# Performance work log

Hardware: AMD Instinct MI355X
Metric: run time of the kernel (lower is better)

The kernel has to match this reference:

```python
import jax, jax.numpy as jnp
import numpy as np

ADMP = 16  # admp_channel


def _backbone(x, Wc, bc):
    # Conv2d(3->256, k=3, stride=2, pad=1) + ReLU stands in for feature_backbone
    y = jax.lax.conv_general_dilated(x, Wc, window_strides=(2, 2),
                                     padding=((1, 1), (1, 1)),
                                     dimension_numbers=('NCHW', 'OIHW', 'NCHW'))
    return jax.nn.relu(y + bc[None, :, None, None])


def _feature_select(feat, k):
    # AdaptiveMaxPool2d(k, return_indices=True) on feat.sum(1); H,W divisible by k
    B, C, H, W = feat.shape
    bh, bw = H // k, W // k
    resp = feat.sum(1)  # [B,H,W]
    r = resp.reshape(B, k, bh, k, bw).transpose(0, 1, 3, 2, 4).reshape(B, k, k, bh * bw)
    loc = jnp.argmax(r, axis=-1)            # local flat index in each bh*bw block
    lr, lc = loc // bw, loc % bw
    rows = jnp.arange(k)[None, :, None] * bh + lr   # [B,k,k]
    cols = jnp.arange(k)[None, None, :] * bw + lc
    return (rows * W + cols).reshape(B, k * k)      # flat indices into H*W


def _mlp(x, W1, b1, W2, b2):
    # Linear -> ReLU -> (Dropout eval = identity) -> Linear
    return jax.nn.relu(x @ W1 + b1) @ W2 + b2


def reference(xA, xB, Wconv, bconv, W1r, b1r, W2r, b2r, W1c, b1c, W2c, b2c):
    fA = _backbone(xA, Wconv, bconv)  # [B,C,H,W]
    fB = _backbone(xB, Wconv, bconv)
    B, C, H, W = fA.shape
    N = H * W
    idxA = _feature_select(fA, ADMP)                       # [B,K]
    fA_flat = fA.reshape(B, C, N)
    fB_flat = fB.reshape(B, C, N)
    desc = jnp.take_along_axis(fA_flat, idxA[:, None, :], axis=2)  # [B,C,K]
    # ||a-b||^2 = ||a||^2 - 2 a.b + ||b||^2 ; fused batched kNN
    dist = ((desc ** 2).sum(1)[:, :, None]
            - 2.0 * jnp.einsum('bck,bcn->bkn', desc, fB_flat)
            + (fB_flat ** 2).sum(1)[:, None, :])           # [B,K,N]
    minidx = jnp.argmin(dist, axis=-1)                     # [B,K]
    # original uses high (==width here since H==W) for both div and mod
    row_A, col_A = idxA // H, idxA % H
    row_B, col_B = minidx // H, minidx % H
    drow = (row_B - row_A).astype(jnp.float32)             # [B,K]
    dcol = (col_A - col_B).astype(jnp.float32)
    out_drow = _mlp(drow, W1r, b1r, W2r, b2r)              # [B,1]
    out_dcol = _mlp(dcol, W1c, b1c, W2c, b2c)
    return jnp.concatenate([out_drow, out_dcol], axis=1)   # [B,2]


def setup_inputs() -> dict:
    key = jax.random.key(0)
    ks = jax.random.split(key, 8)
    K2 = ADMP * ADMP
    return {
        'xA': jax.random.normal(ks[0], (4, 3, 256, 256), jnp.float32),
        'xB': jax.random.normal(ks[1], (4, 3, 256, 256), jnp.float32),
        'Wconv': jax.random.normal(ks[2], (256, 3, 3, 3), jnp.float32) * 0.1,
        'bconv': jnp.zeros((256,), jnp.float32),
        'W1r': jax.random.normal(ks[3], (K2, K2 // 2), jnp.float32) * 0.05,
        'b1r': jnp.zeros((K2 // 2,), jnp.float32),
        'W2r': jax.random.normal(ks[4], (K2 // 2, 1), jnp.float32) * 0.05,
        'b2r': jnp.zeros((1,), jnp.float32),
        'W1c': jax.random.normal(ks[5], (K2, K2 // 2), jnp.float32) * 0.05,
        'b1c': jnp.zeros((K2 // 2,), jnp.float32),
        'W2c': jax.random.normal(ks[6], (K2 // 2, 1), jnp.float32) * 0.05,
        'b2c': jnp.zeros((1,), jnp.float32),
    }
```

## Files before the change

kernel.cpp:

```cpp
#include <hip/hip_runtime.h>
#include <stdint.h>

constexpr int NB   = 4;
constexpr int CIN  = 3;
constexpr int HIN  = 256;
constexpr int COUT = 256;
constexpr int HF   = 128;
constexpr int NF   = HF * HF;
constexpr int KADM = 16;
constexpr int KK   = KADM * KADM;
constexpr int HID  = 128;
constexpr int DFB  = 65536;
constexpr int PX   = 32;
constexpr int NT   = NF / PX;

typedef unsigned short ushort_t;
typedef __attribute__((ext_vector_type(8))) _Float16 f16x8;
typedef __attribute__((ext_vector_type(4))) float    f32x4;

__device__ inline unsigned long long shfl_xor_u64(unsigned long long v, int m) {
    unsigned lo = __shfl_xor((unsigned)v, m, 64);
    unsigned hi = __shfl_xor((unsigned)(v >> 32), m, 64);
    return ((unsigned long long)hi << 32) | lo;
}
__device__ inline unsigned long long shfl_down_u64(unsigned long long v, int off) {
    unsigned lo = __shfl_down((unsigned)v, off, 64);
    unsigned hi = __shfl_down((unsigned)(v >> 32), off, 64);
    return ((unsigned long long)hi << 32) | lo;
}
__device__ inline unsigned long long u64min(unsigned long long a, unsigned long long b) {
    return a < b ? a : b;
}
__device__ inline ushort_t f16bits(_Float16 h) { return __builtin_bit_cast(ushort_t, h); }

__device__ inline int swz(int pix, int c) {
    return pix * 256 + ((((c >> 3) ^ (pix & 7)) << 3) | (c & 7));
}

__device__ inline int dfoff(int w, int chunk, int j, int lane) {
    return (((w * 8 + chunk) * 4 + j) * 64 + lane) * 8;
}

__global__ __launch_bounds__(256) void prep_kernel(
        const float* __restrict__ W, ushort_t* __restrict__ WFh, ushort_t* __restrict__ WFl)
{
    int co = threadIdx.x;
    int w = co >> 6, j = (co >> 4) & 3, la = co & 15;
    #pragma unroll
    for (int q = 0; q < 32; ++q) {
        float v = (q < 27) ? W[co * 27 + q] : 0.f;
        _Float16 h = (_Float16)v;
        _Float16 l = (_Float16)(v - (float)h);
        int lg = q >> 3, e = q & 7;
        int off = ((w * 4 + j) * 64 + lg * 16 + la) * 8 + e;
        WFh[off] = f16bits(h);
        WFl[off] = f16bits(l);
    }
}

__global__ __launch_bounds__(256) void convA_kernel(
        const float* __restrict__ xA,
        const ushort_t* __restrict__ WFh, const ushort_t* __restrict__ WFl,
        const float* __restrict__ bias, float* __restrict__ resp)
{
    __shared__ float    pS[CIN][3][132];
    __shared__ ushort_t Ah[64][40];
    __shared__ ushort_t Al[64][40];
    __shared__ float    redS[4][64];

    int tile = blockIdx.x;
    int b    = blockIdx.y;
    int oh   = tile >> 1;
    int ow0  = (tile & 1) << 6;
    const float* x = xA + (size_t)b * CIN * HIN * HIN;
    int tid = threadIdx.x;

    for (int i = tid; i < CIN * 3 * 129; i += 256) {
        int ci = i / (3 * 129);
        int r2 = i % (3 * 129);
        int kh = r2 / 129, c = r2 % 129;
        int gr = 2 * oh - 1 + kh, gc = 2 * ow0 - 1 + c;
        float v = 0.f;
        if (gr >= 0 && gr < HIN && gc >= 0 && gc < HIN)
            v = x[(size_t)ci * HIN * HIN + (size_t)gr * HIN + gc];
        pS[ci][kh][c] = v;
    }
    __syncthreads();

    {
        int n = tid >> 2, qg = tid & 3;
        unsigned uh[4], ul[4];
        #pragma unroll
        for (int e2 = 0; e2 < 4; ++e2) {
            ushort_t hh[2], ll[2];
            #pragma unroll
            for (int s = 0; s < 2; ++s) {
                int q = qg * 8 + e2 * 2 + s;
                float v = 0.f;
                if (q < 27) {
                    int ci = q / 9, r = (q % 9) / 3, kw = q % 3;
                    v = pS[ci][r][2 * n + kw];
                }
                _Float16 h = (_Float16)v;
                _Float16 l = (_Float16)(v - (float)h);
                hh[s] = f16bits(h); ll[s] = f16bits(l);
            }
            uh[e2] = (unsigned)hh[0] | ((unsigned)hh[1] << 16);
            ul[e2] = (unsigned)ll[0] | ((unsigned)ll[1] << 16);
        }
        *(uint4*)&Ah[n][qg * 8] = *(uint4*)uh;
        *(uint4*)&Al[n][qg * 8] = *(uint4*)ul;
    }
    __syncthreads();

    int lane = tid & 63, w = tid >> 6;
    int la = lane & 15, lg = lane >> 4;
    int wbase = w * 64;

    float bj[4];
    #pragma unroll
    for (int j = 0; j < 4; ++j) bj[j] = bias[wbase + j * 16 + la];

    f16x8 ah[4], al[4], bh[4], bl[4];
    #pragma unroll
    for (int i = 0; i < 4; ++i) {
        ah[i] = *(const f16x8*)&Ah[i * 16 + la][lg * 8];
        al[i] = *(const f16x8*)&Al[i * 16 + la][lg * 8];
    }
    #pragma unroll
    for (int j = 0; j < 4; ++j) {
        int off = ((w * 4 + j) * 64 + lane) * 8;
        bh[j] = *(const f16x8*)&WFh[off];
        bl[j] = *(const f16x8*)&WFl[off];
    }

    f32x4 acc[4][4];
    #pragma unroll
    for (int i = 0; i < 4; ++i)
        #pragma unroll
        for (int j = 0; j < 4; ++j) acc[i][j] = (f32x4)0.f;

    #pragma unroll
    for (int i = 0; i < 4; ++i)
        #pragma unroll
        for (int j = 0; j < 4; ++j) {
            acc[i][j] = __builtin_amdgcn_mfma_f32_16x16x32_f16(ah[i], bh[j], acc[i][j], 0, 0, 0);
            acc[i][j] = __builtin_amdgcn_mfma_f32_16x16x32_f16(al[i], bh[j], acc[i][j], 0, 0, 0);
            acc[i][j] = __builtin_amdgcn_mfma_f32_16x16x32_f16(ah[i], bl[j], acc[i][j], 0, 0, 0);
        }

    float s[4][4];
    #pragma unroll
    for (int i = 0; i < 4; ++i)
        #pragma unroll
        for (int r = 0; r < 4; ++r) s[i][r] = 0.f;

    #pragma unroll
    for (int i = 0; i < 4; ++i)
        #pragma unroll
        for (int j = 0; j < 4; ++j)
            #pragma unroll
            for (int r = 0; r < 4; ++r)
                s[i][r] += fmaxf(acc[i][j][r] + bj[j], 0.f);

    #pragma unroll
    for (int i = 0; i < 4; ++i)
        #pragma unroll
        for (int r = 0; r < 4; ++r) {
            float v = s[i][r];
            v += __shfl_xor(v, 1, 64);
            v += __shfl_xor(v, 2, 64);
            v += __shfl_xor(v, 4, 64);
            v += __shfl_xor(v, 8, 64);
            s[i][r] = v;
        }
    if (la == 0) {
        #pragma unroll
        for (int i = 0; i < 4; ++i)
            #pragma unroll
            for (int r = 0; r < 4; ++r)
                redS[w][i * 16 + lg * 4 + r] = s[i][r];
    }
    __syncthreads();
    if (tid < 64) {
        float tot = redS[0][tid] + redS[1][tid] + redS[2][tid] + redS[3][tid];
        resp[(size_t)b * NF + oh * HF + ow0 + tid] = tot;
    }
}

__global__ __launch_bounds__(256) void select_kernel(
        const float* __restrict__ resp,
        const float* __restrict__ xA, const float* __restrict__ W,
        const float* __restrict__ bias,
        int* __restrict__ idxA,
        ushort_t* __restrict__ dFh, ushort_t* __restrict__ dFl,
        float* __restrict__ normA)
{
    __shared__ float patch[27];
    __shared__ float red[4];
    __shared__ int   sidx;

    int bk = blockIdx.x;
    int b = bk >> 8, k = bk & 255;
    int t = threadIdx.x;

    if (t < 64) {
        int kr = k >> 4, kc = k & 15;
        int lr = t >> 3, lc = t & 7;
        int row = kr * 8 + lr, col = kc * 8 + lc;
        float bv = resp[(size_t)b * NF + (size_t)row * HF + col];
        int best = t;
        for (int off = 32; off > 0; off >>= 1) {
            float ov = __shfl_down(bv, off, 64);
            int   oi = __shfl_down(best, off, 64);
            if (ov > bv || (ov == bv && oi < best)) { bv = ov; best = oi; }
        }
        if (t == 0) {
            int r = kr * 8 + (best >> 3), c = kc * 8 + (best & 7);
            int idx = r * HF + c;
            idxA[bk] = idx;
            sidx = idx;
        }
    }
    __syncthreads();
    int idx = sidx;
    int oh = idx >> 7, ow = idx & 127;

    if (t < 27) {
        int ci = t / 9, kh = (t % 9) / 3, kw = t % 3;
        int ir = oh * 2 - 1 + kh, ic = ow * 2 - 1 + kw;
        float v = 0.f;
        if (ir >= 0 && ir < HIN && ic >= 0 && ic < HIN)
            v = xA[((size_t)b * CIN + ci) * HIN * HIN + (size_t)ir * HIN + ic];
        patch[t] = v;
    }
    __syncthreads();

    float v = bias[t];
    const float* w = &W[t * 27];
    #pragma unroll
    for (int q = 0; q < 27; ++q) v = fmaf(patch[q], w[q], v);
    v = fmaxf(v, 0.f);

    _Float16 h = (_Float16)v;
    _Float16 l = (_Float16)(v - (float)h);
    {
        int wq = k >> 6, j = (k >> 4) & 3, la = k & 15;
        int chunk = t >> 5, lg = (t >> 3) & 3, e = t & 7;
        int off = b * DFB + dfoff(wq, chunk, j, lg * 16 + la) + e;
        dFh[off] = f16bits(h);
        dFl[off] = f16bits(l);
    }

    float s = v * v;
    for (int off = 32; off > 0; off >>= 1) s += __shfl_down(s, off, 64);
    if ((t & 63) == 0) red[t >> 6] = s;
    __syncthreads();
    if (t == 0) normA[bk] = red[0] + red[1] + red[2] + red[3];
}

__device__ inline void load_desc(const ushort_t* __restrict__ dFh,
                                 const ushort_t* __restrict__ dFl,
                                 int w, int chunk, int lane,
                                 f16x8* bh, f16x8* bl)
{
    #pragma unroll
    for (int j = 0; j < 4; ++j) {
        int off = dfoff(w, chunk, j, lane);
        bh[j] = *(const f16x8*)&dFh[off];
        bl[j] = *(const f16x8*)&dFl[off];
    }
}

__device__ inline void knn_chunk(const ushort_t* __restrict__ fH,
                                 const ushort_t* __restrict__ fL,
                                 int la, int lg, int cc,
                                 const f16x8* bh, const f16x8* bl,
                                 f32x4 (&acc)[2][4])
{
    #pragma unroll
    for (int i = 0; i < 2; ++i) {
        f16x8 ah = *(const f16x8*)&fH[swz(i * 16 + la, cc + lg * 8)];
        f16x8 al = *(const f16x8*)&fL[swz(i * 16 + la, cc + lg * 8)];
        __builtin_amdgcn_s_setprio(1);
        #pragma unroll
        for (int j = 0; j < 4; ++j) {
            acc[i][j] = __builtin_amdgcn_mfma_f32_16x16x32_f16(ah, bh[j], acc[i][j], 0, 0, 0);
            acc[i][j] = __builtin_amdgcn_mfma_f32_16x16x32_f16(al, bh[j], acc[i][j], 0, 0, 0);
            acc[i][j] = __builtin_amdgcn_mfma_f32_16x16x32_f16(ah, bl[j], acc[i][j], 0, 0, 0);
        }
        __builtin_amdgcn_s_setprio(0);
    }
}

__global__ __launch_bounds__(256, 4) void fused_kernel(
        const float* __restrict__ xB,
        const ushort_t* __restrict__ WFh, const ushort_t* __restrict__ WFl,
        const float* __restrict__ bias,
        const ushort_t* __restrict__ dFhg, const ushort_t* __restrict__ dFlg,
        const float* __restrict__ normA,
        unsigned long long* __restrict__ scratch)
{
    __shared__ __align__(16) char smem[2 * PX * 256 * 2];
    __shared__ float redS[4][PX];
    __shared__ float nAS[KK];
    __shared__ float nBS[PX];

    float*    pSp = (float*)smem;
    ushort_t* AhP = (ushort_t*)(smem + 2448);
    ushort_t* AlP = (ushort_t*)(smem + 2448 + 2560);
    ushort_t* fH  = (ushort_t*)smem;
    ushort_t* fL  = (ushort_t*)(smem + PX * 256 * 2);

    int tile = blockIdx.x;
    int b    = blockIdx.y;
    int oh   = tile >> 2;
    int ow0  = (tile & 3) << 5;
    const float* x = xB + (size_t)b * CIN * HIN * HIN;
    int tid = threadIdx.x;

    nAS[tid] = normA[b * KK + tid];

    for (int i = tid; i < CIN * 3 * 65; i += 256) {
        int ci = i / (3 * 65);
        int r2 = i % (3 * 65);
        int kh = r2 / 65, c = r2 % 65;
        int gr = 2 * oh - 1 + kh, gc = 2 * ow0 - 1 + c;
        float v = 0.f;
        if (gr >= 0 && gr < HIN && gc >= 0 && gc < HIN)
            v = x[(size_t)ci * HIN * HIN + (size_t)gr * HIN + gc];
        pSp[ci * 204 + kh * 68 + c] = v;
    }
    __syncthreads();

    {
        int n = tid >> 3, qg = tid & 7;
        ushort_t hh[4], ll[4];
        #pragma unroll
        for (int s = 0; s < 4; ++s) {
            int q = qg * 4 + s;
            float v = 0.f;
            if (q < 27) {
                int ci = q / 9, r = (q % 9) / 3, kw = q % 3;
                v = pSp[ci * 204 + r * 68 + 2 * n + kw];
            }
            _Float16 h = (_Float16)v;
            _Float16 l = (_Float16)(v - (float)h);
            hh[s] = f16bits(h); ll[s] = f16bits(l);
        }
        unsigned lo, hi;
        lo = (unsigned)hh[0] | ((unsigned)hh[1] << 16);
        hi = (unsigned)hh[2] | ((unsigned)hh[3] << 16);
        *(uint2*)&AhP[n * 40 + qg * 4] = make_uint2(lo, hi);
        lo = (unsigned)ll[0] | ((unsigned)ll[1] << 16);
        hi = (unsigned)ll[2] | ((unsigned)ll[3] << 16);
        *(uint2*)&AlP[n * 40 + qg * 4] = make_uint2(lo, hi);
    }
    __syncthreads();

    int lane = tid & 63, w = tid >> 6;
    int la = lane & 15, lg = lane >> 4;
    int wbase = w * 64;

    float bj[4];
    #pragma unroll
    for (int j = 0; j < 4; ++j) bj[j] = bias[wbase + j * 16 + la];

    f16x8 cah[2], cal[2], cbh[4], cbl[4];
    #pragma unroll
    for (int i = 0; i < 2; ++i) {
        cah[i] = *(const f16x8*)&AhP[(i * 16 + la) * 40 + lg * 8];
        cal[i] = *(const f16x8*)&AlP[(i * 16 + la) * 40 + lg * 8];
    }
    #pragma unroll
    for (int j = 0; j < 4; ++j) {
        int off = ((w * 4 + j) * 64 + lane) * 8;
        cbh[j] = *(const f16x8*)&WFh[off];
        cbl[j] = *(const f16x8*)&WFl[off];
    }

    f32x4 cacc[2][4];
    #pragma unroll
    for (int i = 0; i < 2; ++i)
        #pragma unroll
        for (int j = 0; j < 4; ++j) cacc[i][j] = (f32x4)0.f;

    #pragma unroll
    for (int i = 0; i < 2; ++i)
        #pragma unroll
        for (int j = 0; j < 4; ++j) {
            cacc[i][j] = __builtin_amdgcn_mfma_f32_16x16x32_f16(cah[i], cbh[j], cacc[i][j], 0, 0, 0);
            cacc[i][j] = __builtin_amdgcn_mfma_f32_16x16x32_f16(cal[i], cbh[j], cacc[i][j], 0, 0, 0);
            cacc[i][j] = __builtin_amdgcn_mfma_f32_16x16x32_f16(cah[i], cbl[j], cacc[i][j], 0, 0, 0);
        }

    __syncthreads();

    float s[2][4];
    #pragma unroll
    for (int i = 0; i < 2; ++i)
        #pragma unroll
        for (int r = 0; r < 4; ++r) s[i][r] = 0.f;

    #pragma unroll
    for (int i = 0; i < 2; ++i) {
        #pragma unroll
        for (int j = 0; j < 4; ++j) {
            int co = wbase + j * 16 + la;
            #pragma unroll
            for (int r = 0; r < 4; ++r) {
                float v = fmaxf(cacc[i][j][r] + bj[j], 0.f);
                _Float16 h = (_Float16)v;
                _Float16 l = (_Float16)(v - (float)h);
                int pix = i * 16 + lg * 4 + r;
                fH[swz(pix, co)] = f16bits(h);
                fL[swz(pix, co)] = f16bits(l);
                s[i][r] = fmaf(v, v, s[i][r]);
            }
        }
    }

    const ushort_t* dFh = dFhg + (size_t)b * DFB;
    const ushort_t* dFl = dFlg + (size_t)b * DFB;
    f16x8 bhA[4], blA[4], bhB[4], blB[4];
    load_desc(dFh, dFl, w, 0, lane, bhA, blA);
    load_desc(dFh, dFl, w, 1, lane, bhB, blB);

    #pragma unroll
    for (int i = 0; i < 2; ++i)
        #pragma unroll
        for (int r = 0; r < 4; ++r) {
            float v = s[i][r];
            v += __shfl_xor(v, 1, 64);
            v += __shfl_xor(v, 2, 64);
            v += __shfl_xor(v, 4, 64);
            v += __shfl_xor(v, 8, 64);
            s[i][r] = v;
        }
    if (la == 0) {
        #pragma unroll
        for (int i = 0; i < 2; ++i)
            #pragma unroll
            for (int r = 0; r < 4; ++r)
                redS[w][i * 16 + lg * 4 + r] = s[i][r];
    }
    __syncthreads();
    if (tid < PX) nBS[tid] = redS[0][tid] + redS[1][tid] + redS[2][tid] + redS[3][tid];
    __syncthreads();

    f32x4 acc[2][4];
    #pragma unroll
    for (int i = 0; i < 2; ++i)
        #pragma unroll
        for (int j = 0; j < 4; ++j) acc[i][j] = (f32x4)0.f;

    knn_chunk(fH, fL, la, lg, 0, bhA, blA, acc);
    load_desc(dFh, dFl, w, 2, lane, bhA, blA);
    knn_chunk(fH, fL, la, lg, 32, bhB, blB, acc);
    load_desc(dFh, dFl, w, 3, lane, bhB, blB);
    knn_chunk(fH, fL, la, lg, 64, bhA, blA, acc);
    load_desc(dFh, dFl, w, 4, lane, bhA, blA);
    knn_chunk(fH, fL, la, lg, 96, bhB, blB, acc);
    load_desc(dFh, dFl, w, 5, lane, bhB, blB);
    knn_chunk(fH, fL, la, lg, 128, bhA, blA, acc);
    load_desc(dFh, dFl, w, 6, lane, bhA, blA);
    knn_chunk(fH, fL, la, lg, 160, bhB, blB, acc);
    load_desc(dFh, dFl, w, 7, lane, bhB, blB);
    knn_chunk(fH, fL, la, lg, 192, bhA, blA, acc);
    knn_chunk(fH, fL, la, lg, 224, bhB, blB, acc);

    float nBv[2][4];
    #pragma unroll
    for (int i = 0; i < 2; ++i) {
        f32x4 t4 = *(const f32x4*)&nBS[i * 16 + lg * 4];
        nBv[i][0] = t4[0]; nBv[i][1] = t4[1]; nBv[i][2] = t4[2]; nBv[i][3] = t4[3];
    }
    int n0 = tile * PX;
    #pragma unroll
    for (int j = 0; j < 4; ++j) {
        int kl = wbase + j * 16 + la;
        float nAv = nAS[kl];
        unsigned long long best = ~0ull;
        #pragma unroll
        for (int i = 0; i < 2; ++i)
            #pragma unroll
            for (int r = 0; r < 4; ++r) {
                int n = n0 + i * 16 + lg * 4 + r;
                float d = fmaf(-2.f, acc[i][j][r], nAv) + nBv[i][r];
                unsigned u = __float_as_uint(d);
                u = (u & 0x80000000u) ? ~u : (u | 0x80000000u);
                unsigned long long key = ((unsigned long long)u << 32) | (unsigned)n;
                best = u64min(best, key);
            }
        best = u64min(best, shfl_xor_u64(best, 16));
        best = u64min(best, shfl_xor_u64(best, 32));
        if (lg == 0)
            scratch[(size_t)(b * KK + kl) * NT + tile] = best;
    }
}

__global__ __launch_bounds__(64) void reduce_kernel(
        const unsigned long long* __restrict__ scratch, int* __restrict__ minN)
{
    int bk = blockIdx.x;
    int t = threadIdx.x;
    const unsigned long long* s = scratch + (size_t)bk * NT;
    unsigned long long best = ~0ull;
    #pragma unroll
    for (int m = 0; m < NT / 64; ++m)
        best = u64min(best, s[t + m * 64]);
    for (int off = 32; off > 0; off >>= 1)
        best = u64min(best, shfl_down_u64(best, off));
    if (t == 0) minN[bk] = (int)(best & 0xffffffffULL);
}

__global__ __launch_bounds__(128) void mlp_kernel(
        const int* __restrict__ idxA, const int* __restrict__ minN,
        const float* __restrict__ W1r, const float* __restrict__ b1r,
        const float* __restrict__ W2r, const float* __restrict__ b2r,
        const float* __restrict__ W1c, const float* __restrict__ b1c,
        const float* __restrict__ W2c, const float* __restrict__ b2c,
        float* __restrict__ out)
{
    __shared__ float xS[KK];
    __shared__ float red[2];
    int blk = blockIdx.x;
    int b = blk >> 1, which = blk & 1;
    int t = threadIdx.x;

    for (int k = t; k < KK; k += 128) {
        int ia = idxA[b * KK + k];
        int nn = minN[b * KK + k];
        int rowA = ia >> 7, colA = ia & 127;
        int rowB = nn >> 7, colB = nn & 127;
        xS[k] = (which == 0) ? (float)(rowB - rowA) : (float)(colA - colB);
    }
    __syncthreads();

    const float* W1 = which ? W1c : W1r;
    const float* b1 = which ? b1c : b1r;
    const float* W2 = which ? W2c : W2r;
    const float* b2 = which ? b2c : b2r;

    float h = b1[t];
    for (int k = 0; k < KK; ++k) h = fmaf(xS[k], W1[k * HID + t], h);
    h = fmaxf(h, 0.f);
    float pv = h * W2[t];
    for (int off = 32; off > 0; off >>= 1) pv += __shfl_down(pv, off, 64);
    if ((t & 63) == 0) red[t >> 6] = pv;
    __syncthreads();
    if (t == 0) out[b * 2 + which] = red[0] + red[1] + b2[0];
}

extern "C" void kernel_launch(void* const* d_in, const int* in_sizes, int n_in,
                              void* d_out, int out_size, void* d_ws, size_t ws_size,
                              hipStream_t stream)
{
    const float* xA  = (const float*)d_in[0];
    const float* xB  = (const float*)d_in[1];
    const float* Wc  = (const float*)d_in[2];
    const float* bc  = (const float*)d_in[3];
    const float* W1r = (const float*)d_in[4];
    const float* b1r = (const float*)d_in[5];
    const float* W2r = (const float*)d_in[6];
    const float* b2r = (const float*)d_in[7];
    const float* W1c = (const float*)d_in[8];
    const float* b1c = (const float*)d_in[9];
    const float* W2c = (const float*)d_in[10];
    const float* b2c = (const float*)d_in[11];
    float* out = (float*)d_out;

    char* ws = (char*)d_ws;
    unsigned long long* scratch = (unsigned long long*)ws; ws += (size_t)NB * KK * NT * 8;
    int*   idxA   = (int*)ws;      ws += (size_t)NB * KK * 4;
    int*   minN   = (int*)ws;      ws += (size_t)NB * KK * 4;
    float* normA  = (float*)ws;    ws += (size_t)NB * KK * 4;
    float* resp   = (float*)ws;    ws += (size_t)NB * NF * 4;
    ushort_t* dFh = (ushort_t*)ws; ws += (size_t)NB * DFB * 2;
    ushort_t* dFl = (ushort_t*)ws; ws += (size_t)NB * DFB * 2;
    ushort_t* WFh = (ushort_t*)ws; ws += (size_t)COUT * 32 * 2;
    ushort_t* WFl = (ushort_t*)ws; ws += (size_t)COUT * 32 * 2;

    prep_kernel  <<<1, 256, 0, stream>>>(Wc, WFh, WFl);
    convA_kernel <<<dim3(256, NB), 256, 0, stream>>>(xA, WFh, WFl, bc, resp);
    select_kernel<<<NB * KK, 256, 0, stream>>>(resp, xA, Wc, bc, idxA, dFh, dFl, normA);
    fused_kernel <<<dim3(NT, NB), 256, 0, stream>>>(xB, WFh, WFl, bc, dFh, dFl,
                                                    normA, scratch);
    reduce_kernel<<<NB * KK, 64, 0, stream>>>(scratch, minN);
    mlp_kernel   <<<8, 128, 0, stream>>>(idxA, minN,
                                         W1r, b1r, W2r, b2r,
                                         W1c, b1c, W2c, b2c, out);
}
```

Measured before the change: 70.79 us.

## Transpose conv MFMA operands, vectorize feature stores, and coalesce kNN scratch layout

The conv MFMA in the fused kernel now swaps operand roles so each lane holds four consecutive channels of one pixel. This lets the bias+ReLU epilogue use packed f16 conversion and 8-byte LDS stores instead of scalar stores, and cuts the norm reduction shuffles. The kNN partial-min scratch is transposed to a [b][tile][k] layout so fused_kernel writes are coalesced. reduce_kernel is rewritten as 32 blocks of 256 threads with shared-memory combining. The conversion switches to round-toward-zero pkrtz, which slightly changes the hi/lo split residuals.

```diff
diff --git a/kernel.cpp b/kernel.cpp
--- a/kernel.cpp
+++ b/kernel.cpp
@@ -16,16 +16,12 @@
 
 typedef unsigned short ushort_t;
 typedef __attribute__((ext_vector_type(8))) _Float16 f16x8;
+typedef __attribute__((ext_vector_type(2))) __fp16   fp16v2;
 typedef __attribute__((ext_vector_type(4))) float    f32x4;
 
 __device__ inline unsigned long long shfl_xor_u64(unsigned long long v, int m) {
     unsigned lo = __shfl_xor((unsigned)v, m, 64);
     unsigned hi = __shfl_xor((unsigned)(v >> 32), m, 64);
-    return ((unsigned long long)hi << 32) | lo;
-}
-__device__ inline unsigned long long shfl_down_u64(unsigned long long v, int off) {
-    unsigned lo = __shfl_down((unsigned)v, off, 64);
-    unsigned hi = __shfl_down((unsigned)(v >> 32), off, 64);
     return ((unsigned long long)hi << 32) | lo;
 }
 __device__ inline unsigned long long u64min(unsigned long long a, unsigned long long b) {
@@ -305,6 +301,7 @@
     __shared__ float redS[4][PX];
     __shared__ float nAS[KK];
     __shared__ float nBS[PX];
+    __shared__ float bS[COUT];
 
     float*    pSp = (float*)smem;
     ushort_t* AhP = (ushort_t*)(smem + 2448);
@@ -320,6 +317,7 @@
     int tid = threadIdx.x;
 
     nAS[tid] = normA[b * KK + tid];
+    bS[tid]  = bias[tid];
 
     for (int i = tid; i < CIN * 3 * 65; i += 256) {
         int ci = i / (3 * 65);
@@ -362,61 +360,59 @@
     int la = lane & 15, lg = lane >> 4;
     int wbase = w * 64;
 
-    float bj[4];
-    #pragma unroll
-    for (int j = 0; j < 4; ++j) bj[j] = bias[wbase + j * 16 + la];
-
-    f16x8 cah[2], cal[2], cbh[4], cbl[4];
-    #pragma unroll
-    for (int i = 0; i < 2; ++i) {
-        cah[i] = *(const f16x8*)&AhP[(i * 16 + la) * 40 + lg * 8];
-        cal[i] = *(const f16x8*)&AlP[(i * 16 + la) * 40 + lg * 8];
-    }
+    f16x8 wah[4], wal[4], pbh[2], pbl[2];
     #pragma unroll
     for (int j = 0; j < 4; ++j) {
         int off = ((w * 4 + j) * 64 + lane) * 8;
-        cbh[j] = *(const f16x8*)&WFh[off];
-        cbl[j] = *(const f16x8*)&WFl[off];
-    }
-
-    f32x4 cacc[2][4];
-    #pragma unroll
-    for (int i = 0; i < 2; ++i)
-        #pragma unroll
-        for (int j = 0; j < 4; ++j) cacc[i][j] = (f32x4)0.f;
-
-    #pragma unroll
-    for (int i = 0; i < 2; ++i)
-        #pragma unroll
-        for (int j = 0; j < 4; ++j) {
-            cacc[i][j] = __builtin_amdgcn_mfma_f32_16x16x32_f16(cah[i], cbh[j], cacc[i][j], 0, 0, 0);
-            cacc[i][j] = __builtin_amdgcn_mfma_f32_16x16x32_f16(cal[i], cbh[j], cacc[i][j], 0, 0, 0);
-            cacc[i][j] = __builtin_amdgcn_mfma_f32_16x16x32_f16(cah[i], cbl[j], cacc[i][j], 0, 0, 0);
-        }
-
-    __syncthreads();
-
-    float s[2][4];
-    #pragma unroll
-    for (int i = 0; i < 2; ++i)
-        #pragma unroll
-        for (int r = 0; r < 4; ++r) s[i][r] = 0.f;
-
+        wah[j] = *(const f16x8*)&WFh[off];
+        wal[j] = *(const f16x8*)&WFl[off];
+    }
     #pragma unroll
     for (int i = 0; i < 2; ++i) {
-        #pragma unroll
-        for (int j = 0; j < 4; ++j) {
-            int co = wbase + j * 16 + la;
-            #pragma unroll
-            for (int r = 0; r < 4; ++r) {
-                float v = fmaxf(cacc[i][j][r] + bj[j], 0.f);
-                _Float16 h = (_Float16)v;
-                _Float16 l = (_Float16)(v - (float)h);
-                int pix = i * 16 + lg * 4 + r;
-                fH[swz(pix, co)] = f16bits(h);
-                fL[swz(pix, co)] = f16bits(l);
-                s[i][r] = fmaf(v, v, s[i][r]);
-            }
+        pbh[i] = *(const f16x8*)&AhP[(i * 16 + la) * 40 + lg * 8];
+        pbl[i] = *(const f16x8*)&AlP[(i * 16 + la) * 40 + lg * 8];
+    }
+
+    f32x4 cacc[4][2];
+    #pragma unroll
+    for (int j = 0; j < 4; ++j)
+        #pragma unroll
+        for (int i = 0; i < 2; ++i) cacc[j][i] = (f32x4)0.f;
+
+    #pragma unroll
+    for (int j = 0; j < 4; ++j)
+        #pragma unroll
+        for (int i = 0; i < 2; ++i) {
+            cacc[j][i] = __builtin_amdgcn_mfma_f32_16x16x32_f16(wah[j], pbh[i], cacc[j][i], 0, 0, 0);
+            cacc[j][i] = __builtin_amdgcn_mfma_f32_16x16x32_f16(wal[j], pbh[i], cacc[j][i], 0, 0, 0);
+            cacc[j][i] = __builtin_amdgcn_mfma_f32_16x16x32_f16(wah[j], pbl[i], cacc[j][i], 0, 0, 0);
+        }
+
+    __syncthreads();
+
+    float s2[2] = {0.f, 0.f};
+    #pragma unroll
+    for (int j = 0; j < 4; ++j) {
+        f32x4 b4 = *(const f32x4*)&bS[wbase + j * 16 + lg * 4];
+        int chunk = (wbase + j * 16 + lg * 4) >> 3;
+        int within = (lg & 1) * 4;
+        #pragma unroll
+        for (int i = 0; i < 2; ++i) {
+            int pix = i * 16 + la;
+            float v0 = fmaxf(cacc[j][i][0] + b4[0], 0.f);
+            float v1 = fmaxf(cacc[j][i][1] + b4[1], 0.f);
+            float v2 = fmaxf(cacc[j][i][2] + b4[2], 0.f);
+            float v3 = fmaxf(cacc[j][i][3] + b4[3], 0.f);
+            s2[i] += v0 * v0 + v1 * v1 + v2 * v2 + v3 * v3;
+            fp16v2 h01 = __builtin_amdgcn_cvt_pkrtz(v0, v1);
+            fp16v2 h23 = __builtin_amdgcn_cvt_pkrtz(v2, v3);
+            fp16v2 l01 = __builtin_amdgcn_cvt_pkrtz(v0 - (float)h01[0], v1 - (float)h01[1]);
+            fp16v2 l23 = __builtin_amdgcn_cvt_pkrtz(v2 - (float)h23[0], v3 - (float)h23[1]);
+            int base = pix * 256 + ((chunk ^ (pix & 7)) << 3) + within;
+            *(uint2*)&fH[base] = make_uint2(__builtin_bit_cast(unsigned, h01),
+                                            __builtin_bit_cast(unsigned, h23));
+            *(uint2*)&fL[base] = make_uint2(__builtin_bit_cast(unsigned, l01),
+                                            __builtin_bit_cast(unsigned, l23));
         }
     }
 
@@ -427,22 +423,11 @@
     load_desc(dFh, dFl, w, 1, lane, bhB, blB);
 
     #pragma unroll
-    for (int i = 0; i < 2; ++i)
-        #pragma unroll
-        for (int r = 0; r < 4; ++r) {
-            float v = s[i][r];
-            v += __shfl_xor(v, 1, 64);
-            v += __shfl_xor(v, 2, 64);
-            v += __shfl_xor(v, 4, 64);
-            v += __shfl_xor(v, 8, 64);
-            s[i][r] = v;
-        }
-    if (la == 0) {
-        #pragma unroll
-        for (int i = 0; i < 2; ++i)
-            #pragma unroll
-            for (int r = 0; r < 4; ++r)
-                redS[w][i * 16 + lg * 4 + r] = s[i][r];
+    for (int i = 0; i < 2; ++i) {
+        float v = s2[i];
+        v += __shfl_xor(v, 16, 64);
+        v += __shfl_xor(v, 32, 64);
+        if (lg == 0) redS[w][i * 16 + la] = v;
     }
     __syncthreads();
     if (tid < PX) nBS[tid] = redS[0][tid] + redS[1][tid] + redS[2][tid] + redS[3][tid];
@@ -476,6 +461,7 @@
         nBv[i][0] = t4[0]; nBv[i][1] = t4[1]; nBv[i][2] = t4[2]; nBv[i][3] = t4[3];
     }
     int n0 = tile * PX;
+    unsigned long long bestj[4];
     #pragma unroll
     for (int j = 0; j < 4; ++j) {
         int kl = wbase + j * 16 + la;
@@ -494,24 +480,38 @@
             }
         best = u64min(best, shfl_xor_u64(best, 16));
         best = u64min(best, shfl_xor_u64(best, 32));
-        if (lg == 0)
-            scratch[(size_t)(b * KK + kl) * NT + tile] = best;
-    }
-}
-
-__global__ __launch_bounds__(64) void reduce_kernel(
+        bestj[j] = best;
+    }
+    unsigned long long key = (lg == 0) ? bestj[0] : (lg == 1) ? bestj[1]
+                           : (lg == 2) ? bestj[2] : bestj[3];
+    int klw = wbase + lg * 16 + la;
+    scratch[((size_t)b * NT + tile) * KK + klw] = key;
+}
+
+__global__ __launch_bounds__(256) void reduce_kernel(
         const unsigned long long* __restrict__ scratch, int* __restrict__ minN)
 {
-    int bk = blockIdx.x;
+    __shared__ unsigned long long part[8][32];
+    int g = blockIdx.x;
+    int b = blockIdx.y;
     int t = threadIdx.x;
-    const unsigned long long* s = scratch + (size_t)bk * NT;
+    int ts = t >> 5, kk = t & 31;
+    int k = g * 32 + kk;
+
     unsigned long long best = ~0ull;
-    #pragma unroll
-    for (int m = 0; m < NT / 64; ++m)
-        best = u64min(best, s[t + m * 64]);
-    for (int off = 32; off > 0; off >>= 1)
-        best = u64min(best, shfl_down_u64(best, off));
-    if (t == 0) minN[bk] = (int)(best & 0xffffffffULL);
+    #pragma unroll 4
+    for (int m = 0; m < NT / 8; ++m) {
+        int tile = m * 8 + ts;
+        best = u64min(best, scratch[((size_t)b * NT + tile) * KK + k]);
+    }
+    part[ts][kk] = best;
+    __syncthreads();
+    if (t < 32) {
+        unsigned long long x = part[0][t];
+        #pragma unroll
+        for (int p = 1; p < 8; ++p) x = u64min(x, part[p][t]);
+        minN[b * KK + g * 32 + t] = (int)(x & 0xffffffffULL);
+    }
 }
 
 __global__ __launch_bounds__(128) void mlp_kernel(
@@ -586,7 +586,7 @@
     select_kernel<<<NB * KK, 256, 0, stream>>>(resp, xA, Wc, bc, idxA, dFh, dFl, normA);
     fused_kernel <<<dim3(NT, NB), 256, 0, stream>>>(xB, WFh, WFl, bc, dFh, dFl,
                                                     normA, scratch);
-    reduce_kernel<<<NB * KK, 64, 0, stream>>>(scratch, minN);
+    reduce_kernel<<<dim3(8, NB), 256, 0, stream>>>(scratch, minN);
     mlp_kernel   <<<8, 128, 0, stream>>>(idxA, minN,
                                          W1r, b1r, W2r, b2r,
                                          W1c, b1c, W2c, b2c, out);
```

Result: no change. 69.96 us (-1.2%).
